# Performance work log

Measured on AMD Instinct MI355X. Metric: run time of the kernel, lower is better.

Reference implementation:

```python
import jax, jax.numpy as jnp
import numpy as np
from jax import lax

SOS = -1
BLANK = 28
MAX_SYMBOLS = 4
T, B, ENC = 128, 32, 1024
VOCAB = 29   # includes blank at index 28
EMB = 320
HID = 320


def setup_inputs() -> dict:
    key = jax.random.key(0)
    ks = jax.random.split(key, 9)
    s = 0.1
    return {
        "x": jax.random.normal(ks[0], (T, B, ENC), jnp.float32),
        "lengths": jax.random.randint(ks[1], (B,), T // 2, T + 1, jnp.int32),
        "embedding": jax.random.normal(ks[2], (VOCAB - 1, EMB), jnp.float32) * s,
        "W_ih": jax.random.normal(ks[3], (4 * HID, EMB), jnp.float32) * s,
        "W_hh": jax.random.normal(ks[4], (4 * HID, HID), jnp.float32) * s,
        "b_ih": jax.random.normal(ks[5], (4 * HID,), jnp.float32) * s,
        "b_hh": jax.random.normal(ks[6], (4 * HID,), jnp.float32) * s,
        "W_joint": jax.random.normal(ks[7], (VOCAB, ENC + HID), jnp.float32) * s,
        "b_joint": jax.random.normal(ks[8], (VOCAB,), jnp.float32) * s,
    }


def _lstm_cell(xe, h, c, W_ih, W_hh, b_ih, b_hh):
    gates = xe @ W_ih.T + h @ W_hh.T + b_ih + b_hh          # [B, 4H]
    i, f, g, o = jnp.split(gates, 4, axis=-1)               # torch gate order
    i, f, o = jax.nn.sigmoid(i), jax.nn.sigmoid(f), jax.nn.sigmoid(o)
    g = jnp.tanh(g)
    c2 = f * c + i * g
    h2 = o * jnp.tanh(c2)
    return h2, c2


def _decode(x, lengths, embedding, W_ih, W_hh, b_ih, b_hh, W_joint, b_joint):
    Tn, Bn, _ = x.shape
    Lmax = Tn * MAX_SYMBOLS
    bidx = jnp.arange(Bn)

    def sym_step(carry, _):
        h, c, last, pos, labels, lps, active = carry
        # pred step: zero embedding for SOS, else embed (label>blank -> label-1)
        adj = jnp.where(last > BLANK, last - 1, last)
        adj = jnp.clip(adj, 0, VOCAB - 2)
        emb = jnp.where((last == SOS)[:, None], 0.0, embedding[adj])  # [B, EMB]
        h2, c2 = _lstm_cell(emb, h, c, W_ih, W_hh, b_ih, b_hh)
        # joint step: concat(enc frame, pred) -> fc -> log_softmax
        f_enc = carry_f                                            # closed over
        logits = jnp.concatenate([f_enc, h2], axis=-1) @ W_joint.T + b_joint
        logp = jax.nn.log_softmax(logits, axis=-1)                 # [B, V]
        idx = jnp.argmax(logp, axis=-1).astype(jnp.int32)
        v = jnp.take_along_axis(logp, idx[:, None].astype(jnp.int32), axis=-1)[:, 0]
        is_blank = idx == BLANK
        emit = active & (~is_blank)
        # commit hidden/label only on non-blank emission (as original)
        h = jnp.where(emit[:, None], h2, h)
        c = jnp.where(emit[:, None], c2, c)
        last = jnp.where(emit, idx, last)
        cur = labels[bidx, pos]
        labels = labels.at[bidx, pos].set(jnp.where(emit, idx, cur))
        lps = lps + jnp.where(active, v, 0.0)
        pos = pos + emit.astype(pos.dtype)
        active = active & (~is_blank)
        return (h, c, last, pos, labels, lps, active), None

    def time_step(carry, inp):
        f_t, t = inp                                              # f_t: [B, ENC]
        h, c, last, pos, labels, lps = carry
        active0 = t < lengths
        global carry_f
        carry_f = f_t
        (h, c, last, pos, labels, lps, _), _ = lax.scan(
            sym_step, (h, c, last, pos, labels, lps, active0), None,
            length=MAX_SYMBOLS)
        return (h, c, last, pos, labels, lps), None

    init = (
        jnp.zeros((Bn, HID), x.dtype),
        jnp.zeros((Bn, HID), x.dtype),
        jnp.full((Bn,), SOS, jnp.int32),
        jnp.zeros((Bn,), jnp.int32),
        jnp.full((Bn, Lmax), -1, jnp.int32),
        jnp.zeros((Bn,), x.dtype),
    )
    (h, c, last, pos, labels, lps), _ = lax.scan(
        time_step, init, (x, jnp.arange(Tn)))
    return labels, pos, lps


def reference(x, lengths, embedding, W_ih, W_hh, b_ih, b_hh, W_joint, b_joint):
    # labels: [B, T*MAX_SYMBOLS] int32, padded with -1
    # n_symbols: [B] number of emitted symbols per utterance
    # logp_sum: [B] sum of selected max log-probs over all evaluated decode steps
    labels, n_symbols, logp_sum = _decode(
        x, lengths, embedding, W_ih, W_hh, b_ih, b_hh, W_joint, b_joint)
    return labels, n_symbols, logp_sum
```

## Files before the change

kernel.cpp:

```cpp
#include <hip/hip_runtime.h>
#include <math.h>

typedef unsigned long long u64;
typedef unsigned int u32;

#define BN 32
#define TN 128
#define ENCD 1024
#define HID 320
#define NG 1280
#define VN 29
#define BLANKI 28
#define SLICES 8
#define UPS 40
#define ROWS 160
#define JW 1344
#define JSTR 41
#define XSTRIDE 70
#define NPOLL (7*69)

#define E_OFF   0
#define E_SZ    (TN*BN*VN)
#define P_OFF   (E_OFF + E_SZ)
#define P_SZ    (VN*NG)
#define X_OFF   (P_OFF + P_SZ)
#define X_U64S  (2*BN*SLICES*XSTRIDE)

__device__ __forceinline__ float dot4(float4 a, float4 b) {
    return a.x*b.x + a.y*b.y + a.z*b.z + a.w*b.w;
}
__device__ __forceinline__ u64 aload(const u64* p) {
    return __hip_atomic_load(p, __ATOMIC_RELAXED, __HIP_MEMORY_SCOPE_AGENT);
}
__device__ __forceinline__ void astore(u64* p, u64 v) {
    __hip_atomic_store(p, v, __ATOMIC_RELAXED, __HIP_MEMORY_SCOPE_AGENT);
}

__global__ __launch_bounds__(256) void k_enc(const float* __restrict__ x,
        const float* __restrict__ Wj, const float* __restrict__ bj,
        float* __restrict__ E, u64* __restrict__ xchg)
{
    __shared__ float xl[4][1056];
    const int tid = threadIdx.x;
    const int blk = blockIdx.x;
    const int t = blk >> 3, b0 = (blk & 7) * 4;

    if (tid < 35) xchg[(size_t)blk*35 + tid] = 0ull;

    #pragma unroll
    for (int bb = 0; bb < 4; ++bb) {
        const float4* src = (const float4*)(x + ((size_t)(t*BN + b0 + bb))*ENCD);
        float4 v4 = src[tid];
        ((float4*)&xl[bb][0])[tid + (tid >> 5)] = v4;
    }
    __syncthreads();
    if (tid < 232) {
        const int v = tid >> 3, k8 = tid & 7;
        float a0=0.f, a1=0.f, a2=0.f, a3=0.f;
        const float4* wrow = (const float4*)(Wj + (size_t)v*JW) + k8*32;
        const float4* x0 = ((const float4*)&xl[0][0]) + k8*33;
        const float4* x1 = ((const float4*)&xl[1][0]) + k8*33;
        const float4* x2 = ((const float4*)&xl[2][0]) + k8*33;
        const float4* x3 = ((const float4*)&xl[3][0]) + k8*33;
        #pragma unroll 4
        for (int m = 0; m < 32; ++m) {
            float4 w4 = wrow[m];
            a0 += dot4(w4, x0[m]);
            a1 += dot4(w4, x1[m]);
            a2 += dot4(w4, x2[m]);
            a3 += dot4(w4, x3[m]);
        }
        #pragma unroll
        for (int d = 1; d < 8; d <<= 1) {
            a0 += __shfl_xor(a0, d); a1 += __shfl_xor(a1, d);
            a2 += __shfl_xor(a2, d); a3 += __shfl_xor(a3, d);
        }
        if (k8 == 0) {
            float bjv = bj[v];
            E[((size_t)(t*BN + b0+0))*VN + v] = a0 + bjv;
            E[((size_t)(t*BN + b0+1))*VN + v] = a1 + bjv;
            E[((size_t)(t*BN + b0+2))*VN + v] = a2 + bjv;
            E[((size_t)(t*BN + b0+3))*VN + v] = a3 + bjv;
        }
    }
}

__global__ __launch_bounds__(256) void k_pred(const float* __restrict__ emb,
        const float* __restrict__ Wih, const float* __restrict__ bih,
        const float* __restrict__ bhh, float* __restrict__ P)
{
    __shared__ float el[HID];
    const int tid = threadIdx.x, j = blockIdx.x;
    if (tid < 80) {
        float4 v4 = make_float4(0.f, 0.f, 0.f, 0.f);
        if (j < 28) v4 = ((const float4*)(emb + (size_t)j*HID))[tid];
        ((float4*)el)[tid] = v4;
    }
    __syncthreads();
    #pragma unroll
    for (int q = 0; q < 5; ++q) {
        const int r = q*256 + tid;
        float acc = bih[r] + bhh[r];
        const float4* wrow = (const float4*)(Wih + (size_t)r*HID);
        #pragma unroll 8
        for (int k4 = 0; k4 < 80; ++k4)
            acc += dot4(wrow[k4], ((const float4*)el)[k4]);
        P[(size_t)j*NG + r] = acc;
    }
}

__global__ __launch_bounds__(256, 1) void k_dec(const int* __restrict__ lengths,
        const float* __restrict__ Whh, const float* __restrict__ Wj,
        const float* __restrict__ E, const float* __restrict__ P,
        u64* __restrict__ xchg, float* __restrict__ out)
{
    __shared__ float P_lds[VN*ROWS];
    __shared__ float Wjh[VN*JSTR];
    __shared__ float h_com[HID];
    __shared__ float h2st[HID];
    __shared__ float c_com[UPS];
    __shared__ float c2st[UPS];
    __shared__ float gates[ROWS];
    __shared__ float plog_l[SLICES*VN];
    __shared__ float pad_force[13600];

    const int tid = threadIdx.x;
    const int bid = blockIdx.x;
    const int b = bid & 31, slice = bid >> 5;
    const int rg = tid >> 3, kg = tid & 7;
    const int lane = tid & 63;

    int len = lengths[b];
    if (len > TN) len = TN;
    if (len < 0) {
        pad_force[tid] = (float)tid;
        h_com[tid & 255] = pad_force[(tid*7) & 13599];
    }

    float4 wq[50];
    #pragma unroll
    for (int q = 0; q < 5; ++q) {
        const int r = rg*5 + q;
        const int gt = r / 40, u = r - gt*40;
        const float4* wrow = (const float4*)(Whh + ((size_t)(gt*HID + slice*UPS + u))*HID + kg*40);
        #pragma unroll
        for (int jb = 0; jb < 10; ++jb) wq[q*10 + jb] = wrow[jb];
    }
    for (int i = tid; i < VN*ROWS; i += 256) {
        const int jj = i / ROWS, r = i - jj*ROWS;
        const int gt = r / 40, u = r - gt*40;
        P_lds[i] = P[(size_t)jj*NG + gt*HID + slice*UPS + u];
    }
    for (int i = tid; i < VN*UPS; i += 256) {
        const int v = i / UPS, k = i - v*UPS;
        Wjh[v*JSTR + k] = Wj[(size_t)v*JW + ENCD + slice*UPS + k];
    }
    for (int i = tid; i < HID; i += 256) h_com[i] = 0.f;
    if (tid < UPS) c_com[tid] = 0.f;
    if (slice == 0) for (int i = tid; i < 512; i += 256) out[b*512 + i] = -1.0f;
    __syncthreads();

    float lps = 0.f;
    int pos = 0, jrow = 28, n = 1;
    bool dirty = true;

    for (int t = 0; t < len; ++t) {
        const float Ereg = (lane < VN)
            ? E[((size_t)(t*BN + b))*VN + lane] : -INFINITY;

        for (int s = 0; s < 4; ++s) {
            if (dirty) {
                __syncthreads();
                const int par = n & 1;
                const size_t mybase = ((size_t)(par*BN + b)*SLICES + slice)*XSTRIDE;
                float acc[5] = {0.f, 0.f, 0.f, 0.f, 0.f};
                #pragma unroll
                for (int jb = 0; jb < 10; ++jb) {
                    float4 hv = *(const float4*)(h_com + kg*40 + jb*4);
                    #pragma unroll
                    for (int q = 0; q < 5; ++q) acc[q] += dot4(wq[q*10 + jb], hv);
                }
                #pragma unroll
                for (int q = 0; q < 5; ++q) {
                    acc[q] += __shfl_xor(acc[q], 1);
                    acc[q] += __shfl_xor(acc[q], 2);
                    acc[q] += __shfl_xor(acc[q], 4);
                }
                if (kg == 0) {
                    #pragma unroll
                    for (int q = 0; q < 5; ++q) {
                        const int r = rg*5 + q;
                        gates[r] = acc[q] + P_lds[jrow*ROWS + r];
                    }
                }
                __syncthreads();
                if (tid < 64) {
                    if (tid < UPS) {
                        const float gi = gates[tid],      gf = gates[40+tid];
                        const float gg = gates[80+tid],   go = gates[120+tid];
                        const float ii = 1.f/(1.f+expf(-gi));
                        const float ff = 1.f/(1.f+expf(-gf));
                        const float oo = 1.f/(1.f+expf(-go));
                        const float G  = tanhf(gg);
                        const float c2 = ff*c_com[tid] + ii*G;
                        c2st[tid] = c2;
                        const float h2 = oo * tanhf(c2);
                        h2st[slice*UPS + tid] = h2;
                        const u64 pk = ((u64)(u32)n << 32) | (u64)__float_as_uint(h2);
                        astore(&xchg[mybase + tid], pk);
                    }
                    if (tid < VN) {
                        float pkv[8];
                        #pragma unroll
                        for (int k8 = 0; k8 < 8; ++k8) {
                            float pk = 0.f;
                            #pragma unroll
                            for (int m2 = 0; m2 < 5; ++m2)
                                pk += Wjh[tid*JSTR + k8*5 + m2]
                                    * h2st[slice*UPS + k8*5 + m2];
                            pkv[k8] = pk;
                        }
                        const float pp = ((pkv[0]+pkv[1])+(pkv[2]+pkv[3]))
                                       + ((pkv[4]+pkv[5])+(pkv[6]+pkv[7]));
                        plog_l[slice*VN + tid] = pp;
                        const u64 pk2 = ((u64)(u32)n << 32) | (u64)__float_as_uint(pp);
                        astore(&xchg[mybase + UPS + tid], pk2);
                    }
                } else {
                    const size_t pbase = ((size_t)(par*BN + b)*SLICES)*XSTRIDE;
                    const int i0 = tid - 64;
                    u64* ap[3]; int jj[3], ww[3]; bool need[3];
                    #pragma unroll
                    for (int r = 0; r < 3; ++r) {
                        const int i = i0 + 192*r;
                        need[r] = (i < NPOLL);
                        int j2 = 0, w = 0;
                        if (need[r]) {
                            j2 = i / 69; w = i - j2*69;
                            j2 += (j2 >= slice);
                        }
                        jj[r] = j2; ww[r] = w;
                        ap[r] = (u64*)&xchg[pbase + (size_t)j2*XSTRIDE + w];
                    }
                    int cap = 0;
                    while ((need[0] | need[1] | need[2]) && cap < (1 << 16)) {
                        u64 v[3];
                        #pragma unroll
                        for (int r = 0; r < 3; ++r)
                            if (need[r]) v[r] = aload(ap[r]);
                        #pragma unroll
                        for (int r = 0; r < 3; ++r) {
                            if (need[r] && (u32)(v[r] >> 32) == (u32)n) {
                                const float f = __uint_as_float((u32)v[r]);
                                if (ww[r] < UPS) h2st[jj[r]*UPS + ww[r]] = f;
                                else             plog_l[jj[r]*VN + (ww[r]-UPS)] = f;
                                need[r] = false;
                            }
                        }
                        ++cap;
                    }
                }
                __syncthreads();
                n++;
            }
            float Lv;
            if (lane < VN) {
                float sA = 0.f;
                #pragma unroll
                for (int j2 = 0; j2 < SLICES; ++j2) sA += plog_l[j2*VN + lane];
                Lv = Ereg + sA;
            } else {
                Lv = -INFINITY;
            }
            float m = Lv; int ai = lane;
            #pragma unroll
            for (int d = 1; d < 64; d <<= 1) {
                const float om = __shfl_xor(m, d);
                const int   oi = __shfl_xor(ai, d);
                if (om > m || (om == m && oi < ai)) { m = om; ai = oi; }
            }
            float e = (lane < VN) ? expf(Lv - m) : 0.f;
            #pragma unroll
            for (int d = 1; d < 64; d <<= 1) e += __shfl_xor(e, d);
            lps += -logf(e);

            if (ai == BLANKI) { dirty = false; break; }
            if (slice == 0 && tid == 0) out[b*512 + pos] = (float)ai;
            pos++;
            h_com[tid] = h2st[tid];
            if (tid < 64) h_com[256 + tid] = h2st[256 + tid];
            if (tid < UPS) c_com[tid] = c2st[tid];
            jrow = ai;
            dirty = true;
        }
    }

    if (slice == 0 && tid == 0) {
        out[16384 + b] = (float)pos;
        out[16416 + b] = lps;
    }
}

extern "C" void kernel_launch(void* const* d_in, const int* in_sizes, int n_in,
                              void* d_out, int out_size, void* d_ws, size_t ws_size,
                              hipStream_t stream) {
    const float* x    = (const float*)d_in[0];
    const int* lens   = (const int*)  d_in[1];
    const float* emb  = (const float*)d_in[2];
    const float* Wih  = (const float*)d_in[3];
    const float* Whh  = (const float*)d_in[4];
    const float* bih  = (const float*)d_in[5];
    const float* bhh  = (const float*)d_in[6];
    const float* Wj   = (const float*)d_in[7];
    const float* bj   = (const float*)d_in[8];
    float* out = (float*)d_out;
    float* ws  = (float*)d_ws;

    float* E    = ws + E_OFF;
    float* P    = ws + P_OFF;
    u64*   xchg = (u64*)(ws + X_OFF);

    hipLaunchKernelGGL(k_enc,  dim3(1024), dim3(256), 0, stream, x, Wj, bj, E, xchg);
    hipLaunchKernelGGL(k_pred, dim3(29),   dim3(256), 0, stream, emb, Wih, bih, bhh, P);
    hipLaunchKernelGGL(k_dec,  dim3(256),  dim3(256), 0, stream,
                       lens, Whh, Wj, E, P, xchg, out);
}
```

Before: 1.785 ms.

## Compute recurrent matvec right after exchange and pipeline exchange polling loads

The W_hh·h gate matvec now runs right after the cross-slice exchange, on the freshly gathered h2st, before the argmax. Its result is kept in registers for the next LSTM step. This removes the separate committed h/c buffers, their copies and one block barrier per step. This is valid because the LSTM state only advances after a non-blank commit. The polling loop also issues the next atomic load before checking the previous value, so load latency overlaps the check. The cost is one extra speculative load per poll.

```diff
diff --git a/kernel.cpp b/kernel.cpp
--- a/kernel.cpp
+++ b/kernel.cpp
@@ -116,13 +116,11 @@
 {
     __shared__ float P_lds[VN*ROWS];
     __shared__ float Wjh[VN*JSTR];
-    __shared__ float h_com[HID];
     __shared__ float h2st[HID];
-    __shared__ float c_com[UPS];
     __shared__ float c2st[UPS];
     __shared__ float gates[ROWS];
     __shared__ float plog_l[SLICES*VN];
-    __shared__ float pad_force[13600];
+    __shared__ float pad_force[14400];
 
     const int tid = threadIdx.x;
     const int bid = blockIdx.x;
@@ -134,7 +132,7 @@
     if (len > TN) len = TN;
     if (len < 0) {
         pad_force[tid] = (float)tid;
-        h_com[tid & 255] = pad_force[(tid*7) & 13599];
+        gates[tid & 127] = pad_force[(tid*7) & 14399];
     }
 
     float4 wq[50];
@@ -155,12 +153,12 @@
         const int v = i / UPS, k = i - v*UPS;
         Wjh[v*JSTR + k] = Wj[(size_t)v*JW + ENCD + slice*UPS + k];
     }
-    for (int i = tid; i < HID; i += 256) h_com[i] = 0.f;
-    if (tid < UPS) c_com[tid] = 0.f;
+    if (tid < UPS) c2st[tid] = 0.f;
     if (slice == 0) for (int i = tid; i < 512; i += 256) out[b*512 + i] = -1.0f;
     __syncthreads();
 
     float lps = 0.f;
+    float acc[5] = {0.f, 0.f, 0.f, 0.f, 0.f};
     int pos = 0, jrow = 28, n = 1;
     bool dirty = true;
 
@@ -170,22 +168,8 @@
 
         for (int s = 0; s < 4; ++s) {
             if (dirty) {
-                __syncthreads();
                 const int par = n & 1;
                 const size_t mybase = ((size_t)(par*BN + b)*SLICES + slice)*XSTRIDE;
-                float acc[5] = {0.f, 0.f, 0.f, 0.f, 0.f};
-                #pragma unroll
-                for (int jb = 0; jb < 10; ++jb) {
-                    float4 hv = *(const float4*)(h_com + kg*40 + jb*4);
-                    #pragma unroll
-                    for (int q = 0; q < 5; ++q) acc[q] += dot4(wq[q*10 + jb], hv);
-                }
-                #pragma unroll
-                for (int q = 0; q < 5; ++q) {
-                    acc[q] += __shfl_xor(acc[q], 1);
-                    acc[q] += __shfl_xor(acc[q], 2);
-                    acc[q] += __shfl_xor(acc[q], 4);
-                }
                 if (kg == 0) {
                     #pragma unroll
                     for (int q = 0; q < 5; ++q) {
@@ -202,7 +186,7 @@
                         const float ff = 1.f/(1.f+expf(-gf));
                         const float oo = 1.f/(1.f+expf(-go));
                         const float G  = tanhf(gg);
-                        const float c2 = ff*c_com[tid] + ii*G;
+                        const float c2 = ff*c2st[tid] + ii*G;
                         c2st[tid] = c2;
                         const float h2 = oo * tanhf(c2);
                         h2st[slice*UPS + tid] = h2;
@@ -242,25 +226,46 @@
                         jj[r] = j2; ww[r] = w;
                         ap[r] = (u64*)&xchg[pbase + (size_t)j2*XSTRIDE + w];
                     }
+                    u64 vc[3];
+                    #pragma unroll
+                    for (int r = 0; r < 3; ++r)
+                        if (need[r]) vc[r] = aload(ap[r]);
                     int cap = 0;
                     while ((need[0] | need[1] | need[2]) && cap < (1 << 16)) {
-                        u64 v[3];
+                        u64 vn[3];
                         #pragma unroll
                         for (int r = 0; r < 3; ++r)
-                            if (need[r]) v[r] = aload(ap[r]);
+                            if (need[r]) vn[r] = aload(ap[r]);
                         #pragma unroll
                         for (int r = 0; r < 3; ++r) {
-                            if (need[r] && (u32)(v[r] >> 32) == (u32)n) {
-                                const float f = __uint_as_float((u32)v[r]);
+                            if (need[r] && (u32)(vc[r] >> 32) == (u32)n) {
+                                const float f = __uint_as_float((u32)vc[r]);
                                 if (ww[r] < UPS) h2st[jj[r]*UPS + ww[r]] = f;
                                 else             plog_l[jj[r]*VN + (ww[r]-UPS)] = f;
                                 need[r] = false;
                             }
+                            vc[r] = vn[r];
                         }
                         ++cap;
                     }
                 }
                 __syncthreads();
+                {
+                    float a2[5] = {0.f, 0.f, 0.f, 0.f, 0.f};
+                    #pragma unroll
+                    for (int jb = 0; jb < 10; ++jb) {
+                        float4 hv = *(const float4*)(h2st + kg*40 + jb*4);
+                        #pragma unroll
+                        for (int q = 0; q < 5; ++q) a2[q] += dot4(wq[q*10 + jb], hv);
+                    }
+                    #pragma unroll
+                    for (int q = 0; q < 5; ++q) {
+                        a2[q] += __shfl_xor(a2[q], 1);
+                        a2[q] += __shfl_xor(a2[q], 2);
+                        a2[q] += __shfl_xor(a2[q], 4);
+                        acc[q] = a2[q];
+                    }
+                }
                 n++;
             }
             float Lv;
@@ -287,9 +292,6 @@
             if (ai == BLANKI) { dirty = false; break; }
             if (slice == 0 && tid == 0) out[b*512 + pos] = (float)ai;
             pos++;
-            h_com[tid] = h2st[tid];
-            if (tid < 64) h_com[256 + tid] = h2st[256 + tid];
-            if (tid < UPS) c_com[tid] = c2st[tid];
             jrow = ai;
             dirty = true;
         }
```

Result: slower. 1.982 ms (+11.0%).
